# Performance work log

Measured on AMD Instinct MI355X. Metric: run time of the kernel, lower is better.

Reference implementation:

```python
import jax, jax.numpy as jnp
import numpy as np

# ---- MERU-style Lorentz geometry helpers (space components, implicit time) ----

def _time(x, curv):
    # x: [..., D] space component; time = sqrt(1/curv + ||x||^2)
    return jnp.sqrt(1.0 / curv + jnp.sum(x * x, axis=-1))


def pairwise_dist(x, y, curv, eps=1e-8):
    # Lorentzian inner product for all pairs: <x,y>_L = x.y - x_t*y_t  -> [N, M]
    xt = _time(x, curv)
    yt = _time(y, curv)
    inner = jnp.einsum('nd,md->nm', x, y) - xt[:, None] * yt[None, :]
    c_xyl = -curv * inner  # >= 1 on the hyperboloid
    return jnp.arccosh(jnp.clip(c_xyl, 1.0 + eps, None)) / jnp.sqrt(curv)


def oxy_angle(x, y, curv, eps=1e-8):
    # exterior angle at x of geodesic triangle (origin, x, y); elementwise over batch
    xt = _time(x, curv)
    yt = _time(y, curv)
    c_xyl = curv * (jnp.sum(x * y, axis=-1) - xt * yt)  # <= -1
    acos_numer = yt + c_xyl * xt
    acos_denom = jnp.linalg.norm(x, axis=-1) * jnp.sqrt(jnp.clip(c_xyl * c_xyl - 1.0, 0.0, None))
    acos_input = acos_numer / (acos_denom + eps)
    return jnp.arccos(jnp.clip(acos_input, -1.0 + eps, 1.0 - eps))


def half_aperture(x, curv, min_radius=0.1, eps=1e-6):
    asin_input = 2.0 * min_radius / (jnp.linalg.norm(x, axis=-1) * jnp.sqrt(curv) + eps)
    return jnp.arcsin(jnp.clip(asin_input, -1.0 + eps, 1.0 - eps))


def soft_cross_entropy(logits, target_probs):
    # torch.nn.CrossEntropyLoss with probability targets (rows need not sum to 1)
    return jnp.mean(-jnp.sum(target_probs * jax.nn.log_softmax(logits, axis=-1), axis=-1))


def entailment_loss(fa, fb, curv, eps=1e-6):
    ang = oxy_angle(fa, fb, curv)
    ap = half_aperture(fa, curv, eps=eps)
    return jnp.mean(jnp.clip(ang - ap, 0.0, None))


def setup_inputs() -> dict:
    key = jax.random.key(0)
    k1, k2, k3, k4 = jax.random.split(key, 4)
    B, D = 4096, 512
    return {
        'image_features': jax.random.normal(k1, (B, D), dtype=jnp.float32),
        'dna_features': jax.random.normal(k2, (B, D), dtype=jnp.float32),
        'text_features': jax.random.normal(k3, (B, D), dtype=jnp.float32),
        'labels': jax.random.randint(k4, (B,), 0, 500, dtype=jnp.int64),
        'logit_scale': jnp.float32(10.0),
        'curv': jnp.float32(1.0),
    }


ENTAIL_WEIGHT = 0.2


def reference(image_features, dna_features, text_features, labels, logit_scale, curv):
    # world_size == 1: gathered features == local features
    label_mat = (labels[None, :] == labels[:, None]).astype(jnp.float32)  # [B, B]

    feats = [image_features, dna_features, text_features]  # idx 0=image, 1=dna, 2=text

    contrastive_losses = []
    entail_losses = []
    for ia in range(3):
        for ib in range(3):
            if ia == ib:
                continue
            sim_ab = -pairwise_dist(feats[ia], feats[ib], curv)
            sim_ba = -pairwise_dist(feats[ib], feats[ia], curv)
            contrastive_losses.append(soft_cross_entropy(logit_scale * sim_ab, label_mat))
            contrastive_losses.append(soft_cross_entropy(logit_scale * sim_ba, label_mat))
            # 2D features branch: entailment only for (dna, image) ordering
            if ia == 1 and ib == 0:
                entail_losses.append(entailment_loss(feats[1], feats[0], curv, eps=1e-6))
            elif ia == 0 and ib == 1:
                entail_losses.append(entailment_loss(feats[1], feats[0], curv, eps=1e-6))

    contrastive_total = sum(contrastive_losses) / len(contrastive_losses)
    entail_total = sum(entail_losses) / len(entail_losses)
    total = contrastive_total + ENTAIL_WEIGHT * entail_total
    return total, contrastive_total, entail_total
```

## Files before the change

kernel.cpp:

```cpp
#include <hip/hip_runtime.h>
#include <stdint.h>

#define B_SZ 4096
#define D_SZ 512
#define SHIFT 64.0f

typedef __attribute__((ext_vector_type(4))) float floatx4;
typedef __attribute__((ext_vector_type(2))) long lng2;
typedef unsigned char u8;
typedef unsigned int u32;

#define GLD_LDS16(gp, sp)                                                              \
    __builtin_amdgcn_global_load_lds(                                                  \
        (const __attribute__((address_space(1))) void*)(gp),                           \
        (__attribute__((address_space(3))) void*)(sp), 16, 0, 0)

#define FP8MFMA(accv, av, bv)                                                          \
    accv = __builtin_amdgcn_mfma_f32_16x16x32_fp8_fp8(av, bv, accv, 0, 0, 0)

__global__ __launch_bounds__(256) void prep_kernel(
    const float* __restrict__ img, const float* __restrict__ dna,
    const float* __restrict__ txt, const float* __restrict__ curv_p,
    const int* __restrict__ labels, int* __restrict__ hist,
    u8* __restrict__ f8, float* __restrict__ times,
    float* __restrict__ zero_f, float* __restrict__ ent_partial) {
    __shared__ int lhist[512];
    __shared__ float red[4];
    int t = threadIdx.x;
    int gid = blockIdx.x * 256 + t;
    if (gid < 49155) zero_f[gid] = 0.0f;

    if (blockIdx.x == 0) {
        lhist[t] = 0; lhist[t + 256] = 0;
        __syncthreads();
        for (int n = t; n < B_SZ; n += 256) atomicAdd(&lhist[labels[n]], 1);
        __syncthreads();
        hist[t] = lhist[t]; hist[t + 256] = lhist[t + 256];
    }

    int wave = gid >> 6;
    int lane = t & 63;
    const float* src = (wave < B_SZ) ? img : (wave < 2 * B_SZ) ? dna : txt;
    int row = wave & (B_SZ - 1);
    const float* p = src + row * D_SZ + lane * 8;
    float4 v0 = *(const float4*)(p);
    float4 v1 = *(const float4*)(p + 4);
    float ss = v0.x*v0.x + v0.y*v0.y + v0.z*v0.z + v0.w*v0.w
             + v1.x*v1.x + v1.y*v1.y + v1.z*v1.z + v1.w*v1.w;
    u32 w0 = __builtin_amdgcn_cvt_pk_fp8_f32(v0.x, v0.y, 0, false);
    w0 = __builtin_amdgcn_cvt_pk_fp8_f32(v0.z, v0.w, w0, true);
    u32 w1 = __builtin_amdgcn_cvt_pk_fp8_f32(v1.x, v1.y, 0, false);
    w1 = __builtin_amdgcn_cvt_pk_fp8_f32(v1.z, v1.w, w1, true);
    uint2 pk; pk.x = w0; pk.y = w1;
    int gperm = (lane & 56) | ((lane & 3) << 1) | ((lane >> 2) & 1);
    *(uint2*)(f8 + (size_t)wave * D_SZ + gperm * 8) = pk;

    bool isdna = (wave >= B_SZ) && (wave < 2 * B_SZ);
    float dot = 0.0f, ssy = 0.0f;
    if (isdna) {
        const float* y = img + row * D_SZ + lane * 8;
        float4 y0 = *(const float4*)y, y1 = *(const float4*)(y + 4);
        dot = v0.x*y0.x + v0.y*y0.y + v0.z*y0.z + v0.w*y0.w
            + v1.x*y1.x + v1.y*y1.y + v1.z*y1.z + v1.w*y1.w;
        ssy = y0.x*y0.x + y0.y*y0.y + y0.z*y0.z + y0.w*y0.w
            + y1.x*y1.x + y1.y*y1.y + y1.z*y1.z + y1.w*y1.w;
    }
    #pragma unroll
    for (int m = 1; m < 64; m <<= 1) {
        ss += __shfl_xor(ss, m);
        if (isdna) { dot += __shfl_xor(dot, m); ssy += __shfl_xor(ssy, m); }
    }
    float curv = curv_p[0];
    float ep = 0.0f;
    if (lane == 0) {
        float xt = sqrtf(1.0f / curv + ss);
        times[wave] = xt;
        if (isdna) {
            float yt = sqrtf(1.0f / curv + ssy);
            float nx = sqrtf(ss);
            float c = curv * (dot - xt * yt);
            float numer = yt + c * xt;
            float denom = nx * sqrtf(fmaxf(c * c - 1.0f, 0.0f));
            float ai = numer / (denom + 1e-8f);
            ai = fminf(fmaxf(ai, -1.0f + 1e-8f), 1.0f - 1e-8f);
            float ang = acosf(ai);
            float as_in = 0.2f / (nx * sqrtf(curv) + 1e-6f);
            as_in = fminf(fmaxf(as_in, -1.0f + 1e-6f), 1.0f - 1e-6f);
            float ap = asinf(as_in);
            ep = fmaxf(ang - ap, 0.0f);
        }
    }
    if (blockIdx.x >= 1024 && blockIdx.x < 2048) {
        if (lane == 0) red[t >> 6] = ep;
        __syncthreads();
        if (t == 0) ent_partial[blockIdx.x - 1024] = red[0] + red[1] + red[2] + red[3];
    }
}

__global__ __launch_bounds__(512) void gemm_epi_kernel(
    const u8* __restrict__ f8, const float* __restrict__ times,
    const int* __restrict__ labels,
    const float* __restrict__ ls_p, const float* __restrict__ curv_p,
    float* __restrict__ rsum_e, float* __restrict__ rsum_t,
    float* __restrict__ csum_e, float* __restrict__ csum_t) {
    __shared__ u8 sA[3][256 * 64];
    __shared__ u8 sB[3][128 * 64];

    int z = blockIdx.z;
    int pa = (z == 2) ? 1 : 0;
    int pb = (z == 0) ? 1 : 2;
    const u8* A  = f8 + (size_t)pa * (B_SZ * D_SZ);
    const u8* Bm = f8 + (size_t)pb * (B_SZ * D_SZ);

    int t = threadIdx.x;
    int rowBlk = blockIdx.y * 256;
    int colBlk = blockIdx.x * 128;
    int wave = t >> 6, lane = t & 63;
    int rq  = wave >> 1;
    int chh = wave & 1;

    int lrow = lane >> 2;
    int lch  = (lane & 3) ^ ((lane >> 3) & 3);
    const u8* gA0 = A  + (size_t)(rowBlk + wave * 32 + lrow)      * D_SZ + lch * 16;
    const u8* gA1 = A  + (size_t)(rowBlk + wave * 32 + 16 + lrow) * D_SZ + lch * 16;
    const u8* gB  = Bm + (size_t)(colBlk + wave * 16 + lrow)      * D_SZ + lch * 16;

    int q = lane >> 4, s = lane & 15;
    int slot16 = (q ^ ((s >> 1) & 3)) << 4;
    int aBase = (rq * 64 + s) * 64 + slot16;
    int bBase = (chh * 64 + s) * 64 + slot16;

    floatx4 acc[4][4];
    #pragma unroll
    for (int ii = 0; ii < 4; ++ii)
        #pragma unroll
        for (int j = 0; j < 4; ++j) acc[ii][j] = (floatx4){0.f, 0.f, 0.f, 0.f};

    {
        GLD_LDS16(gA0,      &sA[0][wave * 2048]);
        GLD_LDS16(gA1,      &sA[0][wave * 2048 + 1024]);
        GLD_LDS16(gB,       &sB[0][wave * 1024]);
        GLD_LDS16(gA0 + 64, &sA[1][wave * 2048]);
        GLD_LDS16(gA1 + 64, &sA[1][wave * 2048 + 1024]);
        GLD_LDS16(gB  + 64, &sB[1][wave * 1024]);
    }

    #pragma unroll
    for (int si = 0; si < D_SZ / 64; ++si) {
        const int cur = si % 3;
        const u8* pA = &sA[cur][0];
        const u8* pB = &sB[cur][0];
        if (si < 7) { asm volatile("s_waitcnt vmcnt(3)" ::: "memory"); }
        else        { asm volatile("s_waitcnt vmcnt(0)" ::: "memory"); }
        asm volatile("s_barrier" ::: "memory");

        lng2 a0 = *(const lng2*)(pA + aBase);
        lng2 a1 = *(const lng2*)(pA + aBase + 1024);
        lng2 a2 = *(const lng2*)(pA + aBase + 2048);
        lng2 a3 = *(const lng2*)(pA + aBase + 3072);
        lng2 b0 = *(const lng2*)(pB + bBase);
        lng2 b1 = *(const lng2*)(pB + bBase + 1024);
        if (si < 6) {
            const int nb = (si + 2) % 3;
            const int ko = (si + 2) * 64;
            GLD_LDS16(gA0 + ko, &sA[nb][wave * 2048]);
            GLD_LDS16(gA1 + ko, &sA[nb][wave * 2048 + 1024]);
        }
        asm volatile("s_barrier" ::: "memory");
        __builtin_amdgcn_s_setprio(1);
        FP8MFMA(acc[0][0], a0.x, b0.x); FP8MFMA(acc[0][1], a0.x, b1.x);
        FP8MFMA(acc[1][0], a1.x, b0.x); FP8MFMA(acc[1][1], a1.x, b1.x);
        FP8MFMA(acc[2][0], a2.x, b0.x); FP8MFMA(acc[2][1], a2.x, b1.x);
        FP8MFMA(acc[3][0], a3.x, b0.x); FP8MFMA(acc[3][1], a3.x, b1.x);
        FP8MFMA(acc[0][0], a0.y, b0.y); FP8MFMA(acc[0][1], a0.y, b1.y);
        FP8MFMA(acc[1][0], a1.y, b0.y); FP8MFMA(acc[1][1], a1.y, b1.y);
        FP8MFMA(acc[2][0], a2.y, b0.y); FP8MFMA(acc[2][1], a2.y, b1.y);
        FP8MFMA(acc[3][0], a3.y, b0.y); FP8MFMA(acc[3][1], a3.y, b1.y);
        __builtin_amdgcn_s_setprio(0);
        asm volatile("s_barrier" ::: "memory");

        lng2 b2 = *(const lng2*)(pB + bBase + 2048);
        lng2 b3 = *(const lng2*)(pB + bBase + 3072);
        if (si < 6) {
            const int nb = (si + 2) % 3;
            const int ko = (si + 2) * 64;
            GLD_LDS16(gB + ko, &sB[nb][wave * 1024]);
        }
        asm volatile("s_barrier" ::: "memory");
        __builtin_amdgcn_s_setprio(1);
        FP8MFMA(acc[0][2], a0.x, b2.x); FP8MFMA(acc[0][3], a0.x, b3.x);
        FP8MFMA(acc[1][2], a1.x, b2.x); FP8MFMA(acc[1][3], a1.x, b3.x);
        FP8MFMA(acc[2][2], a2.x, b2.x); FP8MFMA(acc[2][3], a2.x, b3.x);
        FP8MFMA(acc[3][2], a3.x, b2.x); FP8MFMA(acc[3][3], a3.x, b3.x);
        FP8MFMA(acc[0][2], a0.y, b2.y); FP8MFMA(acc[0][3], a0.y, b3.y);
        FP8MFMA(acc[1][2], a1.y, b2.y); FP8MFMA(acc[1][3], a1.y, b3.y);
        FP8MFMA(acc[2][2], a2.y, b2.y); FP8MFMA(acc[2][3], a2.y, b3.y);
        FP8MFMA(acc[3][2], a3.y, b2.y); FP8MFMA(acc[3][3], a3.y, b3.y);
        __builtin_amdgcn_s_setprio(0);
    }

    float ls = ls_p[0];
    float curv = curv_p[0];
    float rsc = rsqrtf(curv);
    float c2 = -ls * rsc;
    float c1 = c2 * 0.69314718f;
    float sh2p = SHIFT * 1.44269504f + c2;
    const float* tA = times + pa * B_SZ;
    const float* tB = times + pb * B_SZ;

    int rowbase = rowBlk + rq * 64;
    int colbase = colBlk + chh * 64;

    float tb[4]; int lb[4]; int mcol[4];
    #pragma unroll
    for (int j = 0; j < 4; ++j) {
        mcol[j] = colbase + j * 16 + s;
        tb[j] = tB[mcol[j]];
        lb[j] = labels[mcol[j]];
    }
    float colE[4] = {0.f, 0.f, 0.f, 0.f}, colT[4] = {0.f, 0.f, 0.f, 0.f};

    float* rsE = rsum_e + z * B_SZ;
    float* rsT = rsum_t + z * B_SZ;
    float* csE = csum_e + z * B_SZ;
    float* csT = csum_t + z * B_SZ;

    #pragma unroll
    for (int ii = 0; ii < 4; ++ii) {
        int nb = rowbase + ii * 16 + q * 4;
        float cta[4]; int la[4];
        #pragma unroll
        for (int r = 0; r < 4; ++r) { cta[r] = curv * tA[nb + r]; la[r] = labels[nb + r]; }
        float re[4] = {0.f, 0.f, 0.f, 0.f}, rt[4] = {0.f, 0.f, 0.f, 0.f};
        #pragma unroll
        for (int j = 0; j < 4; ++j) {
            floatx4 a = acc[ii][j];
            #pragma unroll
            for (int r = 0; r < 4; ++r) {
                float zc = fmaf(-curv, a[r], cta[r] * tb[j]);
                zc = fmaxf(zc, 1.0f + 1e-8f);
                float lz = __log2f(zc);
                float e = __builtin_amdgcn_exp2f(fmaf(c2, lz, sh2p));
                float tl = (la[r] == lb[j]) ? fmaf(c1, lz, c1) : 0.0f;
                re[r] += e; rt[r] += tl;
                colE[j] += e; colT[j] += tl;
            }
        }
        #pragma unroll
        for (int r = 0; r < 4; ++r) {
            #pragma unroll
            for (int m = 1; m <= 8; m <<= 1) {
                re[r] += __shfl_xor(re[r], m);
                rt[r] += __shfl_xor(rt[r], m);
            }
        }
        #pragma unroll
        for (int r = 0; r < 4; ++r) {
            if (s == r) {
                atomicAdd(&rsE[nb + r], re[r]);
                atomicAdd(&rsT[nb + r], rt[r]);
            }
        }
    }
    #pragma unroll
    for (int j = 0; j < 4; ++j) {
        colE[j] += __shfl_xor(colE[j], 16); colE[j] += __shfl_xor(colE[j], 32);
        colT[j] += __shfl_xor(colT[j], 16); colT[j] += __shfl_xor(colT[j], 32);
        if (q == 0) {
            atomicAdd(&csE[mcol[j]], colE[j]);
            atomicAdd(&csT[mcol[j]], colT[j]);
        }
    }
}

__global__ __launch_bounds__(256) void finalize_kernel(
    const float* __restrict__ rsum_e, const float* __restrict__ rsum_t,
    const float* __restrict__ csum_e, const float* __restrict__ csum_t,
    const int* __restrict__ labels, const int* __restrict__ hist,
    const float* __restrict__ ent_partial,
    float* __restrict__ ce_acc, float* __restrict__ ent_acc,
    int* __restrict__ done, float* __restrict__ out) {
    __shared__ float red[4], red2[4];
    int b = blockIdx.x, tid = threadIdx.x;
    int n = b * 256 + tid;
    float Sn = (float)hist[labels[n]];
    float part = 0.0f;
    #pragma unroll
    for (int p = 0; p < 3; ++p) {
        part += Sn * (__logf(rsum_e[p * B_SZ + n]) - SHIFT) - rsum_t[p * B_SZ + n];
        part += Sn * (__logf(csum_e[p * B_SZ + n]) - SHIFT) - csum_t[p * B_SZ + n];
    }
    float ep = (b < 4) ? ent_partial[b * 256 + tid] : 0.0f;
    #pragma unroll
    for (int m = 1; m < 64; m <<= 1) {
        part += __shfl_xor(part, m);
        ep   += __shfl_xor(ep, m);
    }
    if ((tid & 63) == 0) { red[tid >> 6] = part; red2[tid >> 6] = ep; }
    __syncthreads();
    if (tid == 0) {
        atomicAdd(ce_acc, red[0] + red[1] + red[2] + red[3]);
        atomicAdd(ent_acc, red2[0] + red2[1] + red2[2] + red2[3]);
        __threadfence();
        if (atomicAdd(done, 1) == 15) {
            float ce = atomicAdd(ce_acc, 0.0f);
            float ent = atomicAdd(ent_acc, 0.0f);
            float contr = ce / (6.0f * (float)B_SZ);
            ent /= (float)B_SZ;
            out[0] = contr + 0.2f * ent;
            out[1] = contr;
            out[2] = ent;
        }
    }
}

extern "C" void kernel_launch(void* const* d_in, const int* in_sizes, int n_in,
                              void* d_out, int out_size, void* d_ws, size_t ws_size,
                              hipStream_t stream) {
    const float* img    = (const float*)d_in[0];
    const float* dna    = (const float*)d_in[1];
    const float* txt    = (const float*)d_in[2];
    const int*   labels = (const int*)d_in[3];
    const float* ls     = (const float*)d_in[4];
    const float* curv   = (const float*)d_in[5];

    char* ws = (char*)d_ws;
    u8*    f8     = (u8*)ws;
    float* times  = (float*)(ws + 6291456);
    float* rsum_e = (float*)(ws + 6340608);
    float* rsum_t = (float*)(ws + 6389760);
    float* csum_e = (float*)(ws + 6438912);
    float* csum_t = (float*)(ws + 6488064);
    float* ce_acc = (float*)(ws + 6537216);
    float* ent_acc= (float*)(ws + 6537220);
    int*   done   = (int*)  (ws + 6537224);
    float* ent_p  = (float*)(ws + 6537228);
    int*   hist   = (int*)  (ws + 6541324);

    prep_kernel<<<3072, 256, 0, stream>>>(img, dna, txt, curv, labels, hist,
                                          f8, times, rsum_e, ent_p);
    dim3 g(32, 16, 3);
    gemm_epi_kernel<<<g, 512, 0, stream>>>(f8, times, labels, ls, curv,
                                           rsum_e, rsum_t, csum_e, csum_t);
    finalize_kernel<<<16, 256, 0, stream>>>(rsum_e, rsum_t, csum_e, csum_t,
                                            labels, hist, ent_p,
                                            ce_acc, ent_acc, done, (float*)d_out);
}
```

Measured before the change: 168.0 us.

## Shrink GEMM tile to 128x128 with double buffering for higher occupancy

Halves the row tile of the fused FP8 GEMM+epilogue kernel from 256 to 128, doubles the grid, and drops the triple-buffered split-barrier pipeline for a simpler double-buffered loop with one __syncthreads per K step. LDS use drops from 72KB to 32KB and launch bounds request 4 blocks per CU, aiming at more concurrent blocks and better latency hiding. In exchange each block reuses loaded B data less, global traffic per output rises, and the finer-grained barrier and setprio scheduling is gone.

```diff
diff --git a/kernel.cpp b/kernel.cpp
--- a/kernel.cpp
+++ b/kernel.cpp
@@ -97,14 +97,14 @@
     }
 }
 
-__global__ __launch_bounds__(512) void gemm_epi_kernel(
+__global__ __launch_bounds__(512, 4) void gemm_epi_kernel(
     const u8* __restrict__ f8, const float* __restrict__ times,
     const int* __restrict__ labels,
     const float* __restrict__ ls_p, const float* __restrict__ curv_p,
     float* __restrict__ rsum_e, float* __restrict__ rsum_t,
     float* __restrict__ csum_e, float* __restrict__ csum_t) {
-    __shared__ u8 sA[3][256 * 64];
-    __shared__ u8 sB[3][128 * 64];
+    __shared__ u8 sA[2][128 * 64];
+    __shared__ u8 sB[2][128 * 64];
 
     int z = blockIdx.z;
     int pa = (z == 2) ? 1 : 0;
@@ -113,90 +113,57 @@
     const u8* Bm = f8 + (size_t)pb * (B_SZ * D_SZ);
 
     int t = threadIdx.x;
-    int rowBlk = blockIdx.y * 256;
+    int rowBlk = blockIdx.y * 128;
     int colBlk = blockIdx.x * 128;
     int wave = t >> 6, lane = t & 63;
-    int rq  = wave >> 1;
-    int chh = wave & 1;
-
-    int lrow = lane >> 2;
-    int lch  = (lane & 3) ^ ((lane >> 3) & 3);
-    const u8* gA0 = A  + (size_t)(rowBlk + wave * 32 + lrow)      * D_SZ + lch * 16;
-    const u8* gA1 = A  + (size_t)(rowBlk + wave * 32 + 16 + lrow) * D_SZ + lch * 16;
-    const u8* gB  = Bm + (size_t)(colBlk + wave * 16 + lrow)      * D_SZ + lch * 16;
+    int wr = wave >> 1;
+    int wc = wave & 1;
+
+    int chunk = (t & 3) ^ ((t >> 3) & 3);
+    const u8* gA = A  + (size_t)(rowBlk + (t >> 2)) * D_SZ + chunk * 16;
+    const u8* gB = Bm + (size_t)(colBlk + (t >> 2)) * D_SZ + chunk * 16;
 
     int q = lane >> 4, s = lane & 15;
     int slot16 = (q ^ ((s >> 1) & 3)) << 4;
-    int aBase = (rq * 64 + s) * 64 + slot16;
-    int bBase = (chh * 64 + s) * 64 + slot16;
-
-    floatx4 acc[4][4];
-    #pragma unroll
-    for (int ii = 0; ii < 4; ++ii)
+    int aBase = (wr * 32 + s) * 64 + slot16;
+    int bBase = (wc * 64 + s) * 64 + slot16;
+
+    floatx4 acc[2][4];
+    #pragma unroll
+    for (int ii = 0; ii < 2; ++ii)
         #pragma unroll
         for (int j = 0; j < 4; ++j) acc[ii][j] = (floatx4){0.f, 0.f, 0.f, 0.f};
 
     {
-        GLD_LDS16(gA0,      &sA[0][wave * 2048]);
-        GLD_LDS16(gA1,      &sA[0][wave * 2048 + 1024]);
-        GLD_LDS16(gB,       &sB[0][wave * 1024]);
-        GLD_LDS16(gA0 + 64, &sA[1][wave * 2048]);
-        GLD_LDS16(gA1 + 64, &sA[1][wave * 2048 + 1024]);
-        GLD_LDS16(gB  + 64, &sB[1][wave * 1024]);
+        GLD_LDS16(gA, &sA[0][wave * 1024]);
+        GLD_LDS16(gB, &sB[0][wave * 1024]);
     }
 
     #pragma unroll
     for (int si = 0; si < D_SZ / 64; ++si) {
-        const int cur = si % 3;
+        const int cur = si & 1;
+        __syncthreads();
+        if (si < D_SZ / 64 - 1) {
+            const int ko = (si + 1) * 64;
+            GLD_LDS16(gA + ko, &sA[cur ^ 1][wave * 1024]);
+            GLD_LDS16(gB + ko, &sB[cur ^ 1][wave * 1024]);
+        }
         const u8* pA = &sA[cur][0];
         const u8* pB = &sB[cur][0];
-        if (si < 7) { asm volatile("s_waitcnt vmcnt(3)" ::: "memory"); }
-        else        { asm volatile("s_waitcnt vmcnt(0)" ::: "memory"); }
-        asm volatile("s_barrier" ::: "memory");
-
         lng2 a0 = *(const lng2*)(pA + aBase);
         lng2 a1 = *(const lng2*)(pA + aBase + 1024);
-        lng2 a2 = *(const lng2*)(pA + aBase + 2048);
-        lng2 a3 = *(const lng2*)(pA + aBase + 3072);
         lng2 b0 = *(const lng2*)(pB + bBase);
         lng2 b1 = *(const lng2*)(pB + bBase + 1024);
-        if (si < 6) {
-            const int nb = (si + 2) % 3;
-            const int ko = (si + 2) * 64;
-            GLD_LDS16(gA0 + ko, &sA[nb][wave * 2048]);
-            GLD_LDS16(gA1 + ko, &sA[nb][wave * 2048 + 1024]);
-        }
-        asm volatile("s_barrier" ::: "memory");
-        __builtin_amdgcn_s_setprio(1);
-        FP8MFMA(acc[0][0], a0.x, b0.x); FP8MFMA(acc[0][1], a0.x, b1.x);
-        FP8MFMA(acc[1][0], a1.x, b0.x); FP8MFMA(acc[1][1], a1.x, b1.x);
-        FP8MFMA(acc[2][0], a2.x, b0.x); FP8MFMA(acc[2][1], a2.x, b1.x);
-        FP8MFMA(acc[3][0], a3.x, b0.x); FP8MFMA(acc[3][1], a3.x, b1.x);
-        FP8MFMA(acc[0][0], a0.y, b0.y); FP8MFMA(acc[0][1], a0.y, b1.y);
-        FP8MFMA(acc[1][0], a1.y, b0.y); FP8MFMA(acc[1][1], a1.y, b1.y);
-        FP8MFMA(acc[2][0], a2.y, b0.y); FP8MFMA(acc[2][1], a2.y, b1.y);
-        FP8MFMA(acc[3][0], a3.y, b0.y); FP8MFMA(acc[3][1], a3.y, b1.y);
-        __builtin_amdgcn_s_setprio(0);
-        asm volatile("s_barrier" ::: "memory");
-
         lng2 b2 = *(const lng2*)(pB + bBase + 2048);
         lng2 b3 = *(const lng2*)(pB + bBase + 3072);
-        if (si < 6) {
-            const int nb = (si + 2) % 3;
-            const int ko = (si + 2) * 64;
-            GLD_LDS16(gB + ko, &sB[nb][wave * 1024]);
-        }
-        asm volatile("s_barrier" ::: "memory");
-        __builtin_amdgcn_s_setprio(1);
+        FP8MFMA(acc[0][0], a0.x, b0.x); FP8MFMA(acc[0][1], a0.x, b1.x);
         FP8MFMA(acc[0][2], a0.x, b2.x); FP8MFMA(acc[0][3], a0.x, b3.x);
+        FP8MFMA(acc[1][0], a1.x, b0.x); FP8MFMA(acc[1][1], a1.x, b1.x);
         FP8MFMA(acc[1][2], a1.x, b2.x); FP8MFMA(acc[1][3], a1.x, b3.x);
-        FP8MFMA(acc[2][2], a2.x, b2.x); FP8MFMA(acc[2][3], a2.x, b3.x);
-        FP8MFMA(acc[3][2], a3.x, b2.x); FP8MFMA(acc[3][3], a3.x, b3.x);
+        FP8MFMA(acc[0][0], a0.y, b0.y); FP8MFMA(acc[0][1], a0.y, b1.y);
         FP8MFMA(acc[0][2], a0.y, b2.y); FP8MFMA(acc[0][3], a0.y, b3.y);
+        FP8MFMA(acc[1][0], a1.y, b0.y); FP8MFMA(acc[1][1], a1.y, b1.y);
         FP8MFMA(acc[1][2], a1.y, b2.y); FP8MFMA(acc[1][3], a1.y, b3.y);
-        FP8MFMA(acc[2][2], a2.y, b2.y); FP8MFMA(acc[2][3], a2.y, b3.y);
-        FP8MFMA(acc[3][2], a3.y, b2.y); FP8MFMA(acc[3][3], a3.y, b3.y);
-        __builtin_amdgcn_s_setprio(0);
     }
 
     float ls = ls_p[0];
@@ -208,8 +175,8 @@
     const float* tA = times + pa * B_SZ;
     const float* tB = times + pb * B_SZ;
 
-    int rowbase = rowBlk + rq * 64;
-    int colbase = colBlk + chh * 64;
+    int rowbase = rowBlk + wr * 32;
+    int colbase = colBlk + wc * 64;
 
     float tb[4]; int lb[4]; int mcol[4];
     #pragma unroll
@@ -226,7 +193,7 @@
     float* csT = csum_t + z * B_SZ;
 
     #pragma unroll
-    for (int ii = 0; ii < 4; ++ii) {
+    for (int ii = 0; ii < 2; ++ii) {
         int nb = rowbase + ii * 16 + q * 4;
         float cta[4]; int la[4];
         #pragma unroll
@@ -339,7 +306,7 @@
 
     prep_kernel<<<3072, 256, 0, stream>>>(img, dna, txt, curv, labels, hist,
                                           f8, times, rsum_e, ent_p);
-    dim3 g(32, 16, 3);
+    dim3 g(32, 32, 3);
     gemm_epi_kernel<<<g, 512, 0, stream>>>(f8, times, labels, ls, curv,
                                            rsum_e, rsum_t, csum_e, csum_t);
     finalize_kernel<<<16, 256, 0, stream>>>(rsum_e, rsum_t, csum_e, csum_t,
```

Result: no change. 168.1 us (+0.1%).
